# Optimization experiments

Measured on AMD Instinct MI355X. Metric: run time of the kernel, lower is better.

The kernel has to match this reference:

```python
import jax, jax.numpy as jnp
import numpy as np

# dims: N batch, C in-channels, T frames, V joints, H heads, HD per-head dim, O out-channels
N, C, T, V = 32, 64, 256, 25
H, HD, O = 8, 8, 64  # HD = max(C//8, 8)
SCALE = HD ** -0.5
EPS = 1e-5


def setup_inputs() -> dict:
    key = jax.random.key(0)
    ks = jax.random.split(key, 10)
    return {
        "x": jax.random.normal(ks[0], (N, C, T, V), jnp.float32),
        "ln_gamma": jnp.ones((C,), jnp.float32),
        "ln_beta": jnp.zeros((C,), jnp.float32),
        "w_qk": jax.random.normal(ks[1], (C, 2 * H * HD), jnp.float32),  # to_qk init N(0,1)
        "b_qk": jax.random.normal(ks[2], (2 * H * HD,), jnp.float32) * 0.02,
        "shared_topology": jax.random.uniform(ks[3], (H, V, V), jnp.float32),
        "conv_w": jax.random.normal(ks[4], (H, O, C), jnp.float32) * np.sqrt(2.0 / (O * H)),
        "conv_b": jnp.zeros((H, O), jnp.float32),
        "bn_gamma": jnp.full((O,), 1e-6, jnp.float32),
        "bn_beta": jnp.zeros((O,), jnp.float32),
        "bn_mean": jnp.zeros((O,), jnp.float32),
        "bn_var": jnp.ones((O,), jnp.float32),
    }


def reference(x, ln_gamma, ln_beta, w_qk, b_qk, shared_topology,
              conv_w, conv_b, bn_gamma, bn_beta, bn_mean, bn_var):
    # ---- SelfAttention over joints ----
    y = jnp.transpose(x, (0, 2, 3, 1))                 # [N,T,V,C]
    mu = jnp.mean(y, axis=-1, keepdims=True)
    var = jnp.var(y, axis=-1, keepdims=True)
    yn = (y - mu) * jax.lax.rsqrt(var + EPS) * ln_gamma + ln_beta
    qk = yn @ w_qk + b_qk                              # [N,T,V,2*H*HD]
    B = N * T
    q, k = jnp.split(qk.reshape(B, V, 2 * H * HD), 2, axis=-1)
    q = q.reshape(B, V, H, HD).transpose(0, 2, 1, 3)   # [B,H,V,HD]
    k = k.reshape(B, V, H, HD).transpose(0, 2, 1, 3)
    dots = jnp.einsum("bhid,bhjd->bhij", q, k) * SCALE
    attn = jax.nn.softmax(dots, axis=-1).astype(jnp.float32)  # [B,H,V,V]

    # ---- attention-gated graph conv ----
    A = attn * shared_topology[None]                   # [B,H,V,V]
    feat = jnp.transpose(x, (0, 2, 3, 1)).reshape(B, V, C)  # [B,V,C]
    z = jnp.einsum("bhuv,bvc->bhuc", A, feat)          # per-head aggregate [B,H,V,C]
    # fused per-head 1x1 convs + sum over heads
    out = jnp.einsum("bhuc,hoc->buo", z, conv_w) + conv_b.sum(0)  # [B,V,O]
    out = out.reshape(N, T, V, O).transpose(0, 3, 1, 2)           # [N,O,T,V]

    # ---- BatchNorm (inference-mode) + residual + ReLU ----
    g = (bn_gamma * jax.lax.rsqrt(bn_var + EPS))[None, :, None, None]
    b = (bn_beta - bn_mean * bn_gamma * jax.lax.rsqrt(bn_var + EPS))[None, :, None, None]
    out = out * g + b
    out = jax.nn.relu(out + x)  # down is identity (in_c == out_c)
    return out
```

## Files before the change

kernel.cpp:

```cpp
#include <hip/hip_runtime.h>
#include <math.h>

#define SCALE_L2E 0.51006972157f
#define EPSV 1e-5f

typedef __attribute__((ext_vector_type(8))) short bf16x8;
typedef __attribute__((ext_vector_type(4))) float f32x4;
typedef __attribute__((ext_vector_type(16))) float f32x16;
typedef __attribute__((ext_vector_type(4))) int i32x4;
typedef __attribute__((ext_vector_type(2))) int i32x2;

static __device__ __forceinline__ unsigned short bfh(float f) {
    return (unsigned short)(__builtin_bit_cast(unsigned int, f) >> 16);
}
static __device__ __forceinline__ int pack2(float lo, float hi) {
    return __builtin_amdgcn_perm(__builtin_bit_cast(unsigned int, hi),
                                 __builtin_bit_cast(unsigned int, lo), 0x07060302u);
}
#define LGKM0() __asm__ __volatile__("s_waitcnt lgkmcnt(0)" ::: "memory")
#define MFMA16(a, b, c) __builtin_amdgcn_mfma_f32_16x16x32_bf16((a), (b), (c), 0, 0, 0)

__global__ void prep_kernel(const float* __restrict__ w_qk,
                            const float* __restrict__ conv_w,
                            const float* __restrict__ conv_b,
                            const float* __restrict__ bn_g, const float* __restrict__ bn_b,
                            const float* __restrict__ bn_m, const float* __restrict__ bn_v,
                            unsigned short* __restrict__ ws) {
    int i = blockIdx.x * 256 + threadIdx.x;
    if (i < 8192) {
        int f = i >> 9, rem = i & 511, l = rem >> 3, j = rem & 7;
        int nt = f >> 1, ks = f & 1;
        int k = ks * 32 + (l >> 4) * 8 + j;
        int nn = nt * 16 + (l & 15);
        ws[i] = bfh(w_qk[k * 128 + nn]);
    } else if (i < 40960) {
        int i2 = i - 8192;
        int g = i2 >> 9, rem = i2 & 511, l = rem >> 3, j = rem & 7;
        int h = g >> 3, nt = (g >> 1) & 3, ks = g & 1;
        int c = ks * 32 + (l >> 4) * 8 + j;
        int o = nt * 16 + (l & 15);
        ws[i] = bfh(conv_w[h * 4096 + o * 64 + c]);
    } else if (i < 41024) {
        int o = i - 40960;
        float gv = bn_g[o] * rsqrtf(bn_v[o] + EPSV);
        float bb = bn_b[o] - bn_m[o] * gv;
        float cb = 0.f;
        for (int h = 0; h < 8; h++) cb += conv_b[h * 64 + o];
        float* wsf = (float*)(ws + 40960);
        wsf[o] = gv;
        wsf[64 + o] = bb + cb * gv;
    }
}

__global__ __launch_bounds__(256, 2)
void sagc_kernel(const float* __restrict__ x,
                 const float* __restrict__ ln_g, const float* __restrict__ ln_b,
                 const float* __restrict__ b_qk,
                 const float* __restrict__ topo,
                 const unsigned short* __restrict__ ws,
                 float* __restrict__ out)
{
    __shared__ __align__(16) unsigned char smem[36864];
    const int tid = threadIdx.x;
    const int lane = tid & 63, wv = tid >> 6;
    const int l15 = lane & 15, quad = lane >> 4;
    const int r32 = lane & 31, hi = lane >> 5;

    unsigned char* my = smem + wv * 9216;
    unsigned short* qbuf = (unsigned short*)my;
    unsigned short* kbuf = (unsigned short*)(my + 1536);
    unsigned char*  fwb  = my;
    unsigned char*  pb0  = my + 4096;
    unsigned char*  pb1  = my + 6656;

    unsigned char* xbS = smem + 4096;
    unsigned char* ynS = smem + 8192;

    const unsigned short* wqk = ws;
    const unsigned short* w2f = ws + 8192;
    const float* bnA = (const float*)(ws + 40960);
    const float* bnB = bnA + 64;

    const int tile = blockIdx.x;
    const int n = tile >> 8, t = tile & 255;
    const float* xg = x + (size_t)n * 409600 + (size_t)t * 25;
    float* og = out + (size_t)n * 409600 + (size_t)t * 25;

    const int hp = wv;

    {
        const int rl = lane >> 3, cp = lane & 7;
        const int v = wv * 8 + rl;
        const bool okv = (v < 25);
        float xv[8];
        const float* xc = xg + v;
        #pragma unroll
        for (int j = 0; j < 8; j++)
            xv[j] = okv ? xc[(cp * 8 + j) * 6400] : 0.f;
        float s = 0.f, ss = 0.f;
        #pragma unroll
        for (int j = 0; j < 8; j++) { s += xv[j]; ss += xv[j] * xv[j]; }
        s  += __shfl_xor(s, 1);  s += __shfl_xor(s, 2);  s += __shfl_xor(s, 4);
        ss += __shfl_xor(ss, 1); ss += __shfl_xor(ss, 2); ss += __shfl_xor(ss, 4);
        float mu = s * 0.015625f;
        float rs = rsqrtf(ss * 0.015625f - mu * mu + EPSV);
        f32x4 ga = *(const f32x4*)&ln_g[cp * 8];
        f32x4 gb = *(const f32x4*)&ln_g[cp * 8 + 4];
        f32x4 ba = *(const f32x4*)&ln_b[cp * 8];
        f32x4 bb = *(const f32x4*)&ln_b[cp * 8 + 4];
        i32x4 px, py;
        #pragma unroll
        for (int q = 0; q < 4; q++) {
            float a0 = xv[2 * q], a1 = xv[2 * q + 1];
            float g0 = (2 * q < 4) ? ga[2 * q] : gb[2 * q - 4];
            float g1 = (2 * q + 1 < 4) ? ga[2 * q + 1] : gb[2 * q - 3];
            float b0 = (2 * q < 4) ? ba[2 * q] : bb[2 * q - 4];
            float b1 = (2 * q + 1 < 4) ? ba[2 * q + 1] : bb[2 * q - 3];
            float y0 = okv ? ((a0 - mu) * rs * g0 + b0) : 0.f;
            float y1 = okv ? ((a1 - mu) * rs * g1 + b1) : 0.f;
            px[q] = pack2(a0, a1);
            py[q] = pack2(y0, y1);
        }
        const int blk = cp ^ (v & 7);
        *(i32x4*)(xbS + v * 128 + blk * 16) = px;
        *(i32x4*)(ynS + v * 128 + blk * 16) = py;
    }
    __syncthreads();

    bf16x8 xa[2][2], yna[2][2];
    #pragma unroll
    for (int mt = 0; mt < 2; mt++)
        #pragma unroll
        for (int ks = 0; ks < 2; ks++) {
            int row = mt * 16 + l15;
            int blk = (ks * 4 + quad) ^ (row & 7);
            xa[mt][ks]  = *(const bf16x8*)(xbS + row * 128 + blk * 16);
            yna[mt][ks] = *(const bf16x8*)(ynS + row * 128 + blk * 16);
        }
    __syncthreads();

    f32x4 acc[2][4];
    #pragma unroll
    for (int mt = 0; mt < 2; mt++)
        #pragma unroll
        for (int nt = 0; nt < 4; nt++)
            acc[mt][nt] = (f32x4){0.f, 0.f, 0.f, 0.f};

    const f32x4 z4 = {0.f, 0.f, 0.f, 0.f};
    const bf16x8 z8 = {0, 0, 0, 0, 0, 0, 0, 0};
    const f32x16 z16 = {0.f,0.f,0.f,0.f,0.f,0.f,0.f,0.f,0.f,0.f,0.f,0.f,0.f,0.f,0.f,0.f};

    const int sw4 = (l15 >> 2) & 3;
    unsigned char* w0p = fwb + ((((quad >> 1) ^ sw4)) << 4) + (quad & 1) * 8;
    unsigned char* w1p = fwb + (((((quad >> 1) ^ sw4)) ^ 2) << 4) + (quad & 1) * 8;
    unsigned char* brp = fwb + l15 * 64 + ((quad ^ sw4) << 4);

    const int uc = (r32 < 25) ? r32 : 24;

    auto softmax_store = [&](f32x16& dd, const float* tp, unsigned char* Pb) {
        dd[12] = hi ? -3e30f : dd[12];
        dd[13] = -3e30f; dd[14] = -3e30f; dd[15] = -3e30f;
        float t8[8];
        #pragma unroll
        for (int r = 0; r < 8; r++) t8[r] = fmaxf(dd[r], dd[r + 8]);
        #pragma unroll
        for (int r = 0; r < 4; r++) t8[r] = fmaxf(t8[r], t8[r + 4]);
        float m = fmaxf(fmaxf(t8[0], t8[1]), fmaxf(t8[2], t8[3]));
        m = fmaxf(m, __shfl_xor(m, 32));
        float s0 = 0.f, s1 = 0.f, s2 = 0.f, s3 = 0.f;
        #pragma unroll
        for (int r = 0; r < 16; r += 4) {
            dd[r]     = __builtin_amdgcn_exp2f(dd[r] - m);     s0 += dd[r];
            dd[r + 1] = __builtin_amdgcn_exp2f(dd[r + 1] - m); s1 += dd[r + 1];
            dd[r + 2] = __builtin_amdgcn_exp2f(dd[r + 2] - m); s2 += dd[r + 2];
            dd[r + 3] = __builtin_amdgcn_exp2f(dd[r + 3] - m); s3 += dd[r + 3];
        }
        float s = (s0 + s1) + (s2 + s3);
        s += __shfl_xor(s, 32);
        float inv = __builtin_amdgcn_rcpf(s);
        #pragma unroll
        for (int r = 0; r < 16; r++) dd[r] = dd[r] * inv * tp[r];
        if (r32 < 25) {
            unsigned char* rowp = Pb + r32 * 80 + hi * 8;
            *(i32x2*)(rowp +  0) = (i32x2){pack2(dd[0], dd[1]),   pack2(dd[2], dd[3])};
            *(i32x2*)(rowp + 16) = (i32x2){pack2(dd[4], dd[5]),   pack2(dd[6], dd[7])};
            *(i32x2*)(rowp + 32) = (i32x2){pack2(dd[8], dd[9]),   pack2(dd[10], dd[11])};
            *(i32x2*)(rowp + 48) = (i32x2){pack2(dd[12], dd[13]), pack2(dd[14], dd[15])};
        }
    };

    auto topo_gather = [&](int h, float (&tp)[16]) {
        const float* tb = topo + h * 625 + uc * 25 + hi * 4;
        #pragma unroll
        for (int r = 0; r < 16; r++) {
            int off = (r < 12) ? ((r & 3) + (r >> 2) * 8)
                    : (r == 12 ? (hi ? 0 : 24) : 0);
            tp[r] = tb[off];
        }
    };

    #pragma unroll
    for (int tsel = 0; tsel < 2; tsel++) {
        int nt = tsel ? (4 + hp) : hp;
        bf16x8 b0 = *(const bf16x8*)&wqk[(nt * 2 + 0) * 512 + lane * 8];
        bf16x8 b1 = *(const bf16x8*)&wqk[(nt * 2 + 1) * 512 + lane * 8];
        float bias = b_qk[(tsel ? 64 : 0) + hp * 16 + l15];
        unsigned short* buf = tsel ? kbuf : qbuf;
        #pragma unroll
        for (int mt = 0; mt < 2; mt++) {
            f32x4 d = MFMA16(yna[mt][0], b0, z4);
            d = MFMA16(yna[mt][1], b1, d);
            #pragma unroll
            for (int r = 0; r < 4; r++) {
                int u = mt * 16 + quad * 4 + r;
                if (u < 25) {
                    float val = d[r] + bias;
                    if (!tsel) val *= SCALE_L2E;
                    buf[u * 24 + l15] = bfh(val);
                }
            }
        }
    }

    float tp0[16];
    topo_gather(hp * 2, tp0);
    LGKM0();

    f32x16 p0, p1;
    {
        bf16x8 ak = z8, bq = z8;
        if (hi == 0) {
            ak = *(const bf16x8*)&kbuf[r32 * 24 + 0];
            bq = *(const bf16x8*)&qbuf[r32 * 24 + 0];
        }
        p0 = __builtin_amdgcn_mfma_f32_32x32x16_bf16(ak, bq, z16, 0, 0, 0);
    }
    float tp1[16];
    topo_gather(hp * 2 + 1, tp1);
    {
        bf16x8 ak = z8, bq = z8;
        if (hi == 0) {
            ak = *(const bf16x8*)&kbuf[r32 * 24 + 8];
            bq = *(const bf16x8*)&qbuf[r32 * 24 + 8];
        }
        p1 = __builtin_amdgcn_mfma_f32_32x32x16_bf16(ak, bq, z16, 0, 0, 0);
    }
    softmax_store(p0, tp0, pb0);
    softmax_store(p1, tp1, pb1);

    bf16x8 w2e[8];
    #pragma unroll
    for (int nt = 0; nt < 4; nt++) {
        int h = hp * 2;
        w2e[2 * nt]     = *(const bf16x8*)&w2f[((h * 4 + nt) * 2 + 0) * 512 + lane * 8];
        w2e[2 * nt + 1] = *(const bf16x8*)&w2f[((h * 4 + nt) * 2 + 1) * 512 + lane * 8];
    }
    #pragma unroll
    for (int nt = 0; nt < 4; nt++) {
        f32x4 dw0 = MFMA16(xa[0][0], w2e[2 * nt], z4);
        dw0 = MFMA16(xa[0][1], w2e[2 * nt + 1], dw0);
        f32x4 dw1 = MFMA16(xa[1][0], w2e[2 * nt], z4);
        dw1 = MFMA16(xa[1][1], w2e[2 * nt + 1], dw1);
        i32x2 q0 = {pack2(dw0[0], dw0[1]), pack2(dw0[2], dw0[3])};
        i32x2 q1 = {pack2(dw1[0], dw1[1]), pack2(dw1[2], dw1[3])};
        *(i32x2*)(w0p + nt * 1024 + l15 * 64) = q0;
        *(i32x2*)(w1p + nt * 1024 + l15 * 64) = q1;
    }
    bf16x8 w2o[8];
    #pragma unroll
    for (int nt = 0; nt < 4; nt++) {
        int h = hp * 2 + 1;
        w2o[2 * nt]     = *(const bf16x8*)&w2f[((h * 4 + nt) * 2 + 0) * 512 + lane * 8];
        w2o[2 * nt + 1] = *(const bf16x8*)&w2f[((h * 4 + nt) * 2 + 1) * 512 + lane * 8];
    }
    LGKM0();

    {
        bf16x8 ag0 = *(const bf16x8*)(pb0 + l15 * 80 + quad * 16);
        bf16x8 ag1 = *(const bf16x8*)(pb0 + 1280 + l15 * 80 + quad * 16);
        #pragma unroll
        for (int nt = 0; nt < 4; nt++) {
            bf16x8 br = *(const bf16x8*)(brp + nt * 1024);
            acc[0][nt] = MFMA16(ag0, br, acc[0][nt]);
            acc[1][nt] = MFMA16(ag1, br, acc[1][nt]);
        }
    }

    #pragma unroll
    for (int nt = 0; nt < 4; nt++) {
        f32x4 dw0 = MFMA16(xa[0][0], w2o[2 * nt], z4);
        dw0 = MFMA16(xa[0][1], w2o[2 * nt + 1], dw0);
        f32x4 dw1 = MFMA16(xa[1][0], w2o[2 * nt], z4);
        dw1 = MFMA16(xa[1][1], w2o[2 * nt + 1], dw1);
        i32x2 q0 = {pack2(dw0[0], dw0[1]), pack2(dw0[2], dw0[3])};
        i32x2 q1 = {pack2(dw1[0], dw1[1]), pack2(dw1[2], dw1[3])};
        *(i32x2*)(w0p + nt * 1024 + l15 * 64) = q0;
        *(i32x2*)(w1p + nt * 1024 + l15 * 64) = q1;
    }
    LGKM0();

    {
        bf16x8 ag0 = *(const bf16x8*)(pb1 + l15 * 80 + quad * 16);
        bf16x8 ag1 = *(const bf16x8*)(pb1 + 1280 + l15 * 80 + quad * 16);
        #pragma unroll
        for (int nt = 0; nt < 4; nt++) {
            bf16x8 br = *(const bf16x8*)(brp + nt * 1024);
            acc[0][nt] = MFMA16(ag0, br, acc[0][nt]);
            acc[1][nt] = MFMA16(ag1, br, acc[1][nt]);
        }
    }

    __syncthreads();
    {
        float* red = (float*)smem + wv * 2304;
        #pragma unroll
        for (int mt = 0; mt < 2; mt++)
            #pragma unroll
            for (int nt = 0; nt < 4; nt++)
                *(f32x4*)&red[(nt * 16 + l15) * 36 + mt * 16 + quad * 4] = acc[mt][nt];
    }
    __syncthreads();

    {
        const float* redf = (const float*)smem;
        const int o = wv * 16 + l15;
        const float gA = bnA[o], gB = bnB[o];
        const float* xo = xg + (size_t)o * 6400;
        float* oo = og + (size_t)o * 6400;
        #pragma unroll
        for (int mt = 0; mt < 2; mt++) {
            const int ub = mt * 16 + quad * 4;
            f32x4 s = {0.f, 0.f, 0.f, 0.f};
            #pragma unroll
            for (int w = 0; w < 4; w++)
                s += *(const f32x4*)&redf[w * 2304 + o * 36 + ub];
            if (ub + 3 < 25) {
                f32x4 xr = *(const f32x4*)&xo[ub];
                f32x4 v;
                #pragma unroll
                for (int r = 0; r < 4; r++) v[r] = fmaxf(s[r] * gA + gB + xr[r], 0.f);
                *(f32x4*)&oo[ub] = v;
            } else if (ub < 25) {
                oo[ub] = fmaxf(s[0] * gA + gB + xo[ub], 0.f);
            }
        }
    }
}

extern "C" void kernel_launch(void* const* d_in, const int* in_sizes, int n_in,
                              void* d_out, int out_size, void* d_ws, size_t ws_size,
                              hipStream_t stream) {
    const float* x      = (const float*)d_in[0];
    const float* ln_g   = (const float*)d_in[1];
    const float* ln_b   = (const float*)d_in[2];
    const float* w_qk   = (const float*)d_in[3];
    const float* b_qk   = (const float*)d_in[4];
    const float* topo   = (const float*)d_in[5];
    const float* conv_w = (const float*)d_in[6];
    const float* conv_b = (const float*)d_in[7];
    const float* bn_g   = (const float*)d_in[8];
    const float* bn_b   = (const float*)d_in[9];
    const float* bn_m   = (const float*)d_in[10];
    const float* bn_v   = (const float*)d_in[11];
    float* outp = (float*)d_out;
    unsigned short* wsp = (unsigned short*)d_ws;

    hipLaunchKernelGGL(prep_kernel, dim3(161), dim3(256), 0, stream,
                       w_qk, conv_w, conv_b, bn_g, bn_b, bn_m, bn_v, wsp);
    hipLaunchKernelGGL(sagc_kernel, dim3(8192), dim3(256), 0, stream,
                       x, ln_g, ln_b, b_qk, topo, (const unsigned short*)wsp, outp);
}
```

Measured before the change: 188.8 us.

## Stage raw x tile in LDS with coalesced loads and reuse it for residual

```diff
diff --git a/kernel.cpp b/kernel.cpp
--- a/kernel.cpp
+++ b/kernel.cpp
@@ -6,6 +6,7 @@
 
 typedef __attribute__((ext_vector_type(8))) short bf16x8;
 typedef __attribute__((ext_vector_type(4))) float f32x4;
+typedef __attribute__((ext_vector_type(4), aligned(4))) float f32x4u;
 typedef __attribute__((ext_vector_type(16))) float f32x16;
 typedef __attribute__((ext_vector_type(4))) int i32x4;
 typedef __attribute__((ext_vector_type(2))) int i32x2;
@@ -60,7 +61,7 @@
                  const unsigned short* __restrict__ ws,
                  float* __restrict__ out)
 {
-    __shared__ __align__(16) unsigned char smem[36864];
+    __shared__ __align__(16) unsigned char smem[44288];
     const int tid = threadIdx.x;
     const int lane = tid & 63, wv = tid >> 6;
     const int l15 = lane & 15, quad = lane >> 4;
@@ -73,8 +74,9 @@
     unsigned char*  pb0  = my + 4096;
     unsigned char*  pb1  = my + 6656;
 
-    unsigned char* xbS = smem + 4096;
-    unsigned char* ynS = smem + 8192;
+    float* xrawF = (float*)(smem + 36864);
+    float* mus   = (float*)(smem + 44032);
+    float* rss   = (float*)(smem + 44160);
 
     const unsigned short* wqk = ws;
     const unsigned short* w2f = ws + 8192;
@@ -89,55 +91,87 @@
     const int hp = wv;
 
     {
-        const int rl = lane >> 3, cp = lane & 7;
-        const int v = wv * 8 + rl;
-        const bool okv = (v < 25);
-        float xv[8];
-        const float* xc = xg + v;
-        #pragma unroll
-        for (int j = 0; j < 8; j++)
-            xv[j] = okv ? xc[(cp * 8 + j) * 6400] : 0.f;
+        const int cl = lane & 15, p = lane >> 4;
+        const int c = wv * 16 + cl;
+        const float* xc = xg + (size_t)c * 6400;
+        float* xrow = xrawF + c * 28;
+        f32x4u a = *(const f32x4u*)(xc + 4 * p);
+        *(f32x4*)(xrow + 4 * p) = (f32x4){a[0], a[1], a[2], a[3]};
+        if (p < 2) {
+            f32x4u b = *(const f32x4u*)(xc + 16 + 4 * p);
+            *(f32x4*)(xrow + 16 + 4 * p) = (f32x4){b[0], b[1], b[2], b[3]};
+        } else if (p == 2) {
+            xrow[24] = xc[24];
+        }
+    }
+    __syncthreads();
+
+    {
+        const int vst = wv * 8 + (lane >> 3);
+        const int part = lane & 7;
+        const int vv = (vst < 25) ? vst : 0;
         float s = 0.f, ss = 0.f;
         #pragma unroll
-        for (int j = 0; j < 8; j++) { s += xv[j]; ss += xv[j] * xv[j]; }
-        s  += __shfl_xor(s, 1);  s += __shfl_xor(s, 2);  s += __shfl_xor(s, 4);
+        for (int j = 0; j < 8; j++) {
+            int jj = (j + part) & 7;
+            float a = xrawF[(part * 8 + jj) * 28 + vv];
+            s += a; ss += a * a;
+        }
+        s  += __shfl_xor(s, 1);  s  += __shfl_xor(s, 2);  s  += __shfl_xor(s, 4);
         ss += __shfl_xor(ss, 1); ss += __shfl_xor(ss, 2); ss += __shfl_xor(ss, 4);
-        float mu = s * 0.015625f;
-        float rs = rsqrtf(ss * 0.015625f - mu * mu + EPSV);
-        f32x4 ga = *(const f32x4*)&ln_g[cp * 8];
-        f32x4 gb = *(const f32x4*)&ln_g[cp * 8 + 4];
-        f32x4 ba = *(const f32x4*)&ln_b[cp * 8];
-        f32x4 bb = *(const f32x4*)&ln_b[cp * 8 + 4];
-        i32x4 px, py;
-        #pragma unroll
-        for (int q = 0; q < 4; q++) {
-            float a0 = xv[2 * q], a1 = xv[2 * q + 1];
-            float g0 = (2 * q < 4) ? ga[2 * q] : gb[2 * q - 4];
-            float g1 = (2 * q + 1 < 4) ? ga[2 * q + 1] : gb[2 * q - 3];
-            float b0 = (2 * q < 4) ? ba[2 * q] : bb[2 * q - 4];
-            float b1 = (2 * q + 1 < 4) ? ba[2 * q + 1] : bb[2 * q - 3];
-            float y0 = okv ? ((a0 - mu) * rs * g0 + b0) : 0.f;
-            float y1 = okv ? ((a1 - mu) * rs * g1 + b1) : 0.f;
-            px[q] = pack2(a0, a1);
-            py[q] = pack2(y0, y1);
-        }
-        const int blk = cp ^ (v & 7);
-        *(i32x4*)(xbS + v * 128 + blk * 16) = px;
-        *(i32x4*)(ynS + v * 128 + blk * 16) = py;
+        if (vst < 25 && part == 0) {
+            float mu = s * 0.015625f;
+            mus[vst] = mu;
+            rss[vst] = rsqrtf(ss * 0.015625f - mu * mu + EPSV);
+        }
     }
     __syncthreads();
 
     bf16x8 xa[2][2], yna[2][2];
-    #pragma unroll
-    for (int mt = 0; mt < 2; mt++)
+    {
+        float muv[2], rsv[2], xfv[2][2][8];
+        #pragma unroll
+        for (int mt = 0; mt < 2; mt++) {
+            int v = mt * 16 + l15;
+            bool ok = (v < 25);
+            int vr = ok ? v : 0;
+            muv[mt] = mus[vr];
+            rsv[mt] = rss[vr];
+            #pragma unroll
+            for (int ks = 0; ks < 2; ks++)
+                #pragma unroll
+                for (int j = 0; j < 8; j++) {
+                    int jj = (j + 2 * quad) & 7;
+                    int c = ks * 32 + quad * 8 + jj;
+                    xfv[mt][ks][jj] = ok ? xrawF[c * 28 + v] : 0.f;
+                }
+        }
         #pragma unroll
         for (int ks = 0; ks < 2; ks++) {
-            int row = mt * 16 + l15;
-            int blk = (ks * 4 + quad) ^ (row & 7);
-            xa[mt][ks]  = *(const bf16x8*)(xbS + row * 128 + blk * 16);
-            yna[mt][ks] = *(const bf16x8*)(ynS + row * 128 + blk * 16);
-        }
-    __syncthreads();
+            f32x4 ga = *(const f32x4*)&ln_g[ks * 32 + quad * 8];
+            f32x4 gb = *(const f32x4*)&ln_g[ks * 32 + quad * 8 + 4];
+            f32x4 ba = *(const f32x4*)&ln_b[ks * 32 + quad * 8];
+            f32x4 bb = *(const f32x4*)&ln_b[ks * 32 + quad * 8 + 4];
+            #pragma unroll
+            for (int mt = 0; mt < 2; mt++) {
+                i32x4 px, py;
+                #pragma unroll
+                for (int q = 0; q < 4; q++) {
+                    float a0 = xfv[mt][ks][2 * q], a1 = xfv[mt][ks][2 * q + 1];
+                    float g0 = (q < 2) ? ga[2 * q] : gb[2 * q - 4];
+                    float g1 = (q < 2) ? ga[2 * q + 1] : gb[2 * q - 3];
+                    float b0 = (q < 2) ? ba[2 * q] : bb[2 * q - 4];
+                    float b1 = (q < 2) ? ba[2 * q + 1] : bb[2 * q - 3];
+                    float y0 = (a0 - muv[mt]) * rsv[mt] * g0 + b0;
+                    float y1 = (a1 - muv[mt]) * rsv[mt] * g1 + b1;
+                    px[q] = pack2(a0, a1);
+                    py[q] = pack2(y0, y1);
+                }
+                xa[mt][ks]  = __builtin_bit_cast(bf16x8, px);
+                yna[mt][ks] = __builtin_bit_cast(bf16x8, py);
+            }
+        }
+    }
 
     f32x4 acc[2][4];
     #pragma unroll
@@ -325,7 +359,7 @@
         const float* redf = (const float*)smem;
         const int o = wv * 16 + l15;
         const float gA = bnA[o], gB = bnB[o];
-        const float* xo = xg + (size_t)o * 6400;
+        const float* xo = xrawF + o * 28;
         float* oo = og + (size_t)o * 6400;
         #pragma unroll
         for (int mt = 0; mt < 2; mt++) {
@@ -341,7 +375,7 @@
                 for (int r = 0; r < 4; r++) v[r] = fmaxf(s[r] * gA + gB + xr[r], 0.f);
                 *(f32x4*)&oo[ub] = v;
             } else if (ub < 25) {
-                oo[ub] = fmaxf(s[0] * gA + gB + xo[ub], 0.f);
+                oo[ub] = fmaxf(s[0] * gA + gB + xo[24], 0.f);
             }
         }
     }
```

Measured after the change: 283.8 us. +50.3%, slower.
